# Optimization experiments

Hardware: AMD Instinct MI355X
Metric: run time of the kernel (lower is better)

Reference implementation:

```python
import jax, jax.numpy as jnp
import numpy as np

D_MODEL = 1024
NUM_HEADS = 16
DK = D_MODEL // NUM_HEADS
B, S = 2, 2048


def _init_w(key, out_f, in_f):
    std = 2.0 / (in_f + out_f) ** 0.5
    w = jax.random.truncated_normal(key, -3.0, 3.0, (out_f, in_f), dtype=jnp.float32)
    return w * std


def setup_inputs() -> dict:
    key = jax.random.key(0)
    kx, kq, kk, kv, ko = jax.random.split(key, 5)
    return {
        "x": jax.random.normal(kx, (B, S, D_MODEL), dtype=jnp.float32),
        "Wq": _init_w(kq, D_MODEL, D_MODEL),
        "Wk": _init_w(kk, D_MODEL, D_MODEL),
        "Wv": _init_w(kv, D_MODEL, D_MODEL),
        "Wo": _init_w(ko, D_MODEL, D_MODEL),
    }


def reference(x, Wq, Wk, Wv, Wo):
    b, s, _ = x.shape
    # Linear: einsum('... d_in, d_out d_in -> ... d_out')
    q = jnp.einsum("bsd,ed->bse", x, Wq)
    k = jnp.einsum("bsd,ed->bse", x, Wk)
    v = jnp.einsum("bsd,ed->bse", x, Wv)
    # split heads: [b, s, h*dk] -> [b, h, s, dk]
    q = q.reshape(b, s, NUM_HEADS, DK).transpose(0, 2, 1, 3)
    k = k.reshape(b, s, NUM_HEADS, DK).transpose(0, 2, 1, 3)
    v = v.reshape(b, s, NUM_HEADS, DK).transpose(0, 2, 1, 3)
    scores = jnp.einsum("bhqd,bhkd->bhqk", q, k) / (DK ** 0.5)
    causal = jnp.tril(jnp.ones((s, s), dtype=bool))
    scores = jnp.where(causal, scores, -jnp.inf)
    wei = jax.nn.softmax(scores, axis=-1)
    attn = jnp.einsum("bhqk,bhkd->bhqd", wei, v)
    attn = attn.transpose(0, 2, 1, 3).reshape(b, s, NUM_HEADS * DK)
    return jnp.einsum("bsd,ed->bse", attn, Wo)
```

## Files before the change

### kernel.cpp

```cpp
#include <hip/hip_runtime.h>
#include <hip/hip_bf16.h>
#include <math.h>

typedef __bf16 bf16;
typedef __attribute__((ext_vector_type(8))) __bf16 bf16x8;
typedef __attribute__((ext_vector_type(4))) __bf16 bf16x4;
typedef __attribute__((ext_vector_type(4))) float f32x4;

#define NHEAD 16
#define DKH 64
#define SEQ 2048
#define DMODEL 1024

__device__ __forceinline__ void gl_lds16(const void* g, void* lds) {
  __builtin_amdgcn_global_load_lds(
      (const __attribute__((address_space(1))) unsigned int*)g,
      (__attribute__((address_space(3))) unsigned int*)lds, 16, 0, 0);
}

__global__ void cvt5_kernel(const float* __restrict__ x, const float* __restrict__ wq,
                            const float* __restrict__ wk, const float* __restrict__ wv,
                            const float* __restrict__ wo, bf16* __restrict__ xb,
                            bf16* __restrict__ wqb, bf16* __restrict__ wkb,
                            bf16* __restrict__ wvb, bf16* __restrict__ wob) {
  int i = blockIdx.x * blockDim.x + threadIdx.x;
  const float* src; bf16* dst; int li;
  if (i < 1048576)      { src = x;  dst = xb;  li = i; }
  else if (i < 1310720) { src = wq; dst = wqb; li = i - 1048576; }
  else if (i < 1572864) { src = wk; dst = wkb; li = i - 1310720; }
  else if (i < 1835008) { src = wv; dst = wvb; li = i - 1572864; }
  else                  { src = wo; dst = wob; li = i - 1835008; }
  float4 v = ((const float4*)src)[li];
  bf16x4 o = { (bf16)v.x, (bf16)v.y, (bf16)v.z, (bf16)v.w };
  ((bf16x4*)dst)[li] = o;
}

template<int MODE>
__global__ __launch_bounds__(256) void gemm_nt(const bf16* __restrict__ A,
                                               const bf16* __restrict__ Bw,
                                               float* __restrict__ Cf,
                                               bf16* __restrict__ Cq,
                                               bf16* __restrict__ Ck,
                                               bf16* __restrict__ Cv,
                                               int M, int N, int K) {
  __shared__ __attribute__((aligned(16))) bf16 As[128 * 32];
  __shared__ __attribute__((aligned(16))) bf16 Bs[128 * 32];
  const int t = threadIdx.x;
  const int w = t >> 6, l = t & 63;
  const int wr = w >> 1, wc = w & 1;
  const int lin = blockIdx.y * gridDim.x + blockIdx.x;
  const int cpx = (gridDim.x * gridDim.y) >> 3;
  const int swz = (lin & 7) * cpx + (lin >> 3);
  const int tm = (swz / gridDim.x) * 128, tn = (swz % gridDim.x) * 128;
  const int srow = l >> 2, scol = (l & 3) * 8;
  const int c16 = l & 15, g4 = l >> 4;

  f32x4 acc[4][4];
#pragma unroll
  for (int i = 0; i < 4; ++i)
#pragma unroll
    for (int j = 0; j < 4; ++j) acc[i][j] = f32x4{0.f, 0.f, 0.f, 0.f};

  for (int k0 = 0; k0 < K; k0 += 32) {
#pragma unroll
    for (int j = 0; j < 2; ++j) {
      const int r0 = w * 32 + j * 16;
      gl_lds16(A + (size_t)(tm + r0 + srow) * K + k0 + scol, &As[r0 * 32]);
      gl_lds16(Bw + (size_t)(tn + r0 + srow) * K + k0 + scol, &Bs[r0 * 32]);
    }
    __syncthreads();
    bf16x8 af[4], bfr[4];
#pragma unroll
    for (int i = 0; i < 4; ++i)
      af[i] = *(const bf16x8*)&As[(wr * 64 + i * 16 + c16) * 32 + g4 * 8];
#pragma unroll
    for (int j = 0; j < 4; ++j)
      bfr[j] = *(const bf16x8*)&Bs[(wc * 64 + j * 16 + c16) * 32 + g4 * 8];
#pragma unroll
    for (int i = 0; i < 4; ++i)
#pragma unroll
      for (int j = 0; j < 4; ++j)
        acc[i][j] = __builtin_amdgcn_mfma_f32_16x16x32_bf16(af[i], bfr[j], acc[i][j], 0, 0, 0);
    __syncthreads();
  }

  const int which = tn >> 10;
#pragma unroll
  for (int i = 0; i < 4; ++i) {
    const int row0 = tm + wr * 64 + i * 16 + g4 * 4;
#pragma unroll
    for (int j = 0; j < 4; ++j) {
      const int col = tn + wc * 64 + j * 16 + c16;
      if (MODE == 0) {
#pragma unroll
        for (int r = 0; r < 4; ++r) Cf[(size_t)(row0 + r) * N + col] = acc[i][j][r];
      } else {
        const int lc = col & 1023;
        if (which == 2) {
          const int bb = row0 >> 11, s = row0 & 2047;
          const int hh = lc >> 6, dk = lc & 63;
          bf16x4 o = { (bf16)acc[i][j][0], (bf16)acc[i][j][1],
                       (bf16)acc[i][j][2], (bf16)acc[i][j][3] };
          *(bf16x4*)&Cv[((size_t)(bb * NHEAD + hh) * DKH + dk) * SEQ + s] = o;
        } else {
          bf16* dst = which ? Ck : Cq;
#pragma unroll
          for (int r = 0; r < 4; ++r)
            dst[(size_t)(row0 + r) * DMODEL + lc] = (bf16)acc[i][j][r];
        }
      }
    }
  }
}

__device__ __forceinline__ bf16x8 lds_frag(const bf16* T, int row, int gran) {
  return *(const bf16x8*)&T[row * 64 + ((gran ^ (row & 7)) << 3)];
}

__device__ __forceinline__ f32x4 vmax4(f32x4 a, f32x4 b) {
  return f32x4{ fmaxf(a[0], b[0]), fmaxf(a[1], b[1]),
                fmaxf(a[2], b[2]), fmaxf(a[3], b[3]) };
}

__global__ __launch_bounds__(256) void attn_kernel(const bf16* __restrict__ qb,
                                                   const bf16* __restrict__ kb,
                                                   const bf16* __restrict__ vT,
                                                   bf16* __restrict__ ob) {
  __shared__ __attribute__((aligned(16))) bf16 Kt[2][64 * 64];
  __shared__ __attribute__((aligned(16))) bf16 Vt[2][64 * 64];
  __shared__ __attribute__((aligned(16))) bf16 Pb[4][16 * 64];
  const int w = threadIdx.x >> 6, l = threadIdx.x & 63;
  const int lin = blockIdx.x;
  const int swz = (lin & 7) * 64 + (lin >> 3);
  const int pr = swz & 15, h = (swz >> 4) & 15, b = swz >> 8;
  const int qtA = 31 - pr, qtB = pr;
  const int c16 = l & 15, g4 = l >> 4, r8 = l >> 3;
  const int sg = ((l & 7) ^ (r8 & 7)) * 8;

  const float SC = 0.125f * 1.44269504089f;

  const bf16* kbase = kb + (size_t)b * SEQ * DMODEL + h * DKH;
  const bf16* vbase = vT + (size_t)(b * NHEAD + h) * DKH * SEQ;

  bf16x8 qfA[2], qfB[2];
#pragma unroll
  for (int d = 0; d < 2; ++d) {
    qfA[d] = *(const bf16x8*)(qb + (size_t)(b * SEQ + qtA * 64 + w * 16 + c16) * DMODEL +
                              h * DKH + d * 32 + g4 * 8);
    qfB[d] = *(const bf16x8*)(qb + (size_t)(b * SEQ + qtB * 64 + w * 16 + c16) * DMODEL +
                              h * DKH + d * 32 + g4 * 8);
  }

  auto stage = [&](int buf, int t) {
    const int kt0 = t * 64;
#pragma unroll
    for (int c = 0; c < 2; ++c) {
      const int row = w * 16 + c * 8;
      gl_lds16(kbase + (size_t)(kt0 + row + r8) * DMODEL + sg, &Kt[buf][row * 64]);
      gl_lds16(vbase + (size_t)(row + r8) * SEQ + kt0 + sg, &Vt[buf][row * 64]);
    }
  };

  stage(0, 0);
  __syncthreads();

  float mm = -INFINITY, ll = 0.f;
  f32x4 acc[4];
#pragma unroll
  for (int n = 0; n < 4; ++n) acc[n] = f32x4{0.f, 0.f, 0.f, 0.f};

  const int TA = qtA + 1, TT = TA + qtB + 1;
  const int ql = w * 16 + c16;

  for (int tt = 0; tt < TT; ++tt) {
    const int cur = tt & 1;
    if (tt + 1 < TT) stage(cur ^ 1, (tt + 1 < TA) ? tt + 1 : tt + 1 - TA);
    const bool pA = tt < TA;
    const int t_in = pA ? tt : tt - TA;
    const bool diag = (t_in == (pA ? qtA : qtB));
    const bf16x8 q0 = pA ? qfA[0] : qfB[0];
    const bf16x8 q1 = pA ? qfA[1] : qfB[1];

    f32x4 s[4];
    __builtin_amdgcn_s_setprio(1);
#pragma unroll
    for (int j = 0; j < 4; ++j) {
      bf16x8 kf0 = lds_frag(Kt[cur], j * 16 + c16, g4);
      bf16x8 kf1 = lds_frag(Kt[cur], j * 16 + c16, 4 + g4);
      f32x4 c = f32x4{0.f, 0.f, 0.f, 0.f};
      c = __builtin_amdgcn_mfma_f32_16x16x32_bf16(kf0, q0, c, 0, 0, 0);
      c = __builtin_amdgcn_mfma_f32_16x16x32_bf16(kf1, q1, c, 0, 0, 0);
      s[j] = c * SC;
    }
    __builtin_amdgcn_s_setprio(0);
    if (diag) {
#pragma unroll
      for (int j = 0; j < 4; ++j)
#pragma unroll
        for (int r = 0; r < 4; ++r)
          if (j * 16 + g4 * 4 + r > ql) s[j][r] = -INFINITY;
    }
    f32x4 t01 = vmax4(s[0], s[1]);
    f32x4 t23 = vmax4(s[2], s[3]);
    f32x4 tv = vmax4(t01, t23);
    float v = fmaxf(fmaxf(tv[0], tv[1]), fmaxf(tv[2], tv[3]));
    v = fmaxf(v, __shfl_xor(v, 16));
    v = fmaxf(v, __shfl_xor(v, 32));
    const float mn = fmaxf(mm, v);
    const float scl = __builtin_amdgcn_exp2f(mm - mn);
    f32x4 ps = f32x4{0.f, 0.f, 0.f, 0.f};
#pragma unroll
    for (int j = 0; j < 4; ++j)
#pragma unroll
      for (int r = 0; r < 4; ++r) {
        float p = __builtin_amdgcn_exp2f(s[j][r] - mn);
        s[j][r] = p;
        ps[r] += p;
      }
    float rs = (ps[0] + ps[1]) + (ps[2] + ps[3]);
    rs += __shfl_xor(rs, 16);
    rs += __shfl_xor(rs, 32);
    ll = ll * scl + rs;
    mm = mn;
    bf16* P = &Pb[w][0];
#pragma unroll
    for (int j = 0; j < 4; ++j) {
      const int col = j * 16 + g4 * 4;
      bf16x4 pk = { (bf16)s[j][0], (bf16)s[j][1], (bf16)s[j][2], (bf16)s[j][3] };
      *(bf16x4*)&P[c16 * 64 + (((col >> 3) ^ (c16 & 7)) << 3) + (col & 7)] = pk;
    }
    float sc4[4];
#pragma unroll
    for (int r = 0; r < 4; ++r) sc4[r] = __shfl(scl, g4 * 4 + r);
#pragma unroll
    for (int n = 0; n < 4; ++n)
#pragma unroll
      for (int r = 0; r < 4; ++r) acc[n][r] *= sc4[r];
    bf16x8 pa0 = lds_frag(P, c16, g4);
    bf16x8 pa1 = lds_frag(P, c16, 4 + g4);
    __builtin_amdgcn_s_setprio(1);
#pragma unroll
    for (int n = 0; n < 4; ++n) {
      bf16x8 vf0 = lds_frag(Vt[cur], n * 16 + c16, g4);
      bf16x8 vf1 = lds_frag(Vt[cur], n * 16 + c16, 4 + g4);
      acc[n] = __builtin_amdgcn_mfma_f32_16x16x32_bf16(pa0, vf0, acc[n], 0, 0, 0);
      acc[n] = __builtin_amdgcn_mfma_f32_16x16x32_bf16(pa1, vf1, acc[n], 0, 0, 0);
    }
    __builtin_amdgcn_s_setprio(0);

    if (tt == TA - 1) {
      float ls[4];
#pragma unroll
      for (int r = 0; r < 4; ++r) ls[r] = __shfl(ll, g4 * 4 + r);
#pragma unroll
      for (int n = 0; n < 4; ++n)
#pragma unroll
        for (int r = 0; r < 4; ++r) {
          float o = acc[n][r] / ls[r];
          ob[(size_t)(b * SEQ + qtA * 64 + w * 16 + g4 * 4 + r) * DMODEL +
             h * DKH + n * 16 + c16] = (bf16)o;
          acc[n][r] = 0.f;
        }
      mm = -INFINITY;
      ll = 0.f;
    }
    __syncthreads();
  }

  float ls[4];
#pragma unroll
  for (int r = 0; r < 4; ++r) ls[r] = __shfl(ll, g4 * 4 + r);
#pragma unroll
  for (int n = 0; n < 4; ++n)
#pragma unroll
    for (int r = 0; r < 4; ++r) {
      float o = acc[n][r] / ls[r];
      ob[(size_t)(b * SEQ + qtB * 64 + w * 16 + g4 * 4 + r) * DMODEL +
         h * DKH + n * 16 + c16] = (bf16)o;
    }
}

extern "C" void kernel_launch(void* const* d_in, const int* in_sizes, int n_in,
                              void* d_out, int out_size, void* d_ws, size_t ws_size,
                              hipStream_t stream) {
  const float* x  = (const float*)d_in[0];
  const float* Wq = (const float*)d_in[1];
  const float* Wk = (const float*)d_in[2];
  const float* Wv = (const float*)d_in[3];
  const float* Wo = (const float*)d_in[4];
  float* out = (float*)d_out;
  char* ws = (char*)d_ws;
  const size_t MB = (size_t)1 << 20;

  bf16* xb   = (bf16*)(ws + 0 * MB);
  bf16* wqb  = (bf16*)(ws + 8 * MB);
  bf16* wkb  = (bf16*)(ws + 10 * MB);
  bf16* wvb  = (bf16*)(ws + 12 * MB);
  bf16* wob  = (bf16*)(ws + 14 * MB);
  bf16* qbuf = (bf16*)(ws + 16 * MB);
  bf16* kbuf = (bf16*)(ws + 24 * MB);
  bf16* vTb  = (bf16*)(ws + 32 * MB);
  bf16* abuf = (bf16*)(ws + 40 * MB);

  cvt5_kernel<<<8192, 256, 0, stream>>>(x, Wq, Wk, Wv, Wo, xb, wqb, wkb, wvb, wob);

  gemm_nt<3><<<dim3(3072 / 128, 4096 / 128), 256, 0, stream>>>(
      xb, wqb, nullptr, qbuf, kbuf, vTb, 4096, 3072, 1024);

  attn_kernel<<<dim3(512), 256, 0, stream>>>(qbuf, kbuf, vTb, abuf);

  gemm_nt<0><<<dim3(1024 / 128, 4096 / 128), 256, 0, stream>>>(
      abuf, wob, out, nullptr, nullptr, nullptr, 4096, 1024, 1024);
}
```

Baseline: 194.9 us.

## Widen GEMM K-tile with swizzled LDS and add lazy softmax rescale with MFMA row sums

The GEMM K-step doubles to 64, and its LDS tiles use an XOR swizzle through the shared lds_frag helper. This halves the barrier count and should cut bank conflicts. The attention kernel folds the softmax scale into an FMA before exp2. It rescales the accumulator only when the running max grows past a threshold, checked once per wave. Row sums are computed by MFMA against a ones vector instead of by shuffle reductions, which trades VALU and shuffle work for extra matrix ops and bf16-rounded sums.

Result: faster. 181.8 us (-6.7%).

```diff
diff --git a/kernel.cpp b/kernel.cpp
--- a/kernel.cpp
+++ b/kernel.cpp
@@ -35,6 +35,10 @@
   ((bf16x4*)dst)[li] = o;
 }
 
+__device__ __forceinline__ bf16x8 lds_frag(const bf16* T, int row, int gran) {
+  return *(const bf16x8*)&T[row * 64 + ((gran ^ (row & 7)) << 3)];
+}
+
 template<int MODE>
 __global__ __launch_bounds__(256) void gemm_nt(const bf16* __restrict__ A,
                                                const bf16* __restrict__ Bw,
@@ -43,8 +47,8 @@
                                                bf16* __restrict__ Ck,
                                                bf16* __restrict__ Cv,
                                                int M, int N, int K) {
-  __shared__ __attribute__((aligned(16))) bf16 As[128 * 32];
-  __shared__ __attribute__((aligned(16))) bf16 Bs[128 * 32];
+  __shared__ __attribute__((aligned(16))) bf16 As[128 * 64];
+  __shared__ __attribute__((aligned(16))) bf16 Bs[128 * 64];
   const int t = threadIdx.x;
   const int w = t >> 6, l = t & 63;
   const int wr = w >> 1, wc = w & 1;
@@ -52,8 +56,8 @@
   const int cpx = (gridDim.x * gridDim.y) >> 3;
   const int swz = (lin & 7) * cpx + (lin >> 3);
   const int tm = (swz / gridDim.x) * 128, tn = (swz % gridDim.x) * 128;
-  const int srow = l >> 2, scol = (l & 3) * 8;
-  const int c16 = l & 15, g4 = l >> 4;
+  const int c16 = l & 15, g4 = l >> 4, r8 = l >> 3;
+  const int sg = ((l & 7) ^ (r8 & 7)) * 8;
 
   f32x4 acc[4][4];
 #pragma unroll
@@ -61,26 +65,29 @@
 #pragma unroll
     for (int j = 0; j < 4; ++j) acc[i][j] = f32x4{0.f, 0.f, 0.f, 0.f};
 
-  for (int k0 = 0; k0 < K; k0 += 32) {
-#pragma unroll
-    for (int j = 0; j < 2; ++j) {
-      const int r0 = w * 32 + j * 16;
-      gl_lds16(A + (size_t)(tm + r0 + srow) * K + k0 + scol, &As[r0 * 32]);
-      gl_lds16(Bw + (size_t)(tn + r0 + srow) * K + k0 + scol, &Bs[r0 * 32]);
+  for (int k0 = 0; k0 < K; k0 += 64) {
+#pragma unroll
+    for (int c = 0; c < 4; ++c) {
+      const int r0 = w * 32 + c * 8;
+      gl_lds16(A + (size_t)(tm + r0 + r8) * K + k0 + sg, &As[r0 * 64]);
+      gl_lds16(Bw + (size_t)(tn + r0 + r8) * K + k0 + sg, &Bs[r0 * 64]);
     }
     __syncthreads();
-    bf16x8 af[4], bfr[4];
-#pragma unroll
-    for (int i = 0; i < 4; ++i)
-      af[i] = *(const bf16x8*)&As[(wr * 64 + i * 16 + c16) * 32 + g4 * 8];
-#pragma unroll
-    for (int j = 0; j < 4; ++j)
-      bfr[j] = *(const bf16x8*)&Bs[(wc * 64 + j * 16 + c16) * 32 + g4 * 8];
-#pragma unroll
-    for (int i = 0; i < 4; ++i)
+#pragma unroll
+    for (int h = 0; h < 2; ++h) {
+      bf16x8 af[4], bfr[4];
+#pragma unroll
+      for (int i = 0; i < 4; ++i)
+        af[i] = lds_frag(As, wr * 64 + i * 16 + c16, h * 4 + g4);
 #pragma unroll
       for (int j = 0; j < 4; ++j)
-        acc[i][j] = __builtin_amdgcn_mfma_f32_16x16x32_bf16(af[i], bfr[j], acc[i][j], 0, 0, 0);
+        bfr[j] = lds_frag(Bs, wc * 64 + j * 16 + c16, h * 4 + g4);
+#pragma unroll
+      for (int i = 0; i < 4; ++i)
+#pragma unroll
+        for (int j = 0; j < 4; ++j)
+          acc[i][j] = __builtin_amdgcn_mfma_f32_16x16x32_bf16(af[i], bfr[j], acc[i][j], 0, 0, 0);
+    }
     __syncthreads();
   }
 
@@ -111,10 +118,6 @@
       }
     }
   }
-}
-
-__device__ __forceinline__ bf16x8 lds_frag(const bf16* T, int row, int gran) {
-  return *(const bf16x8*)&T[row * 64 + ((gran ^ (row & 7)) << 3)];
 }
 
 __device__ __forceinline__ f32x4 vmax4(f32x4 a, f32x4 b) {
@@ -137,7 +140,11 @@
   const int c16 = l & 15, g4 = l >> 4, r8 = l >> 3;
   const int sg = ((l & 7) ^ (r8 & 7)) * 8;
 
-  const float SC = 0.125f * 1.44269504089f;
+  const float SC2 = 0.125f * 1.44269504089f;
+  const float THR = 8.0f / SC2;
+
+  const bf16 oneb = (bf16)1.0f;
+  const bf16x8 ones = { oneb, oneb, oneb, oneb, oneb, oneb, oneb, oneb };
 
   const bf16* kbase = kb + (size_t)b * SEQ * DMODEL + h * DKH;
   const bf16* vbase = vT + (size_t)(b * NHEAD + h) * DKH * SEQ;
@@ -164,7 +171,8 @@
   stage(0, 0);
   __syncthreads();
 
-  float mm = -INFINITY, ll = 0.f;
+  float mm = -INFINITY;
+  f32x4 lsum4 = f32x4{0.f, 0.f, 0.f, 0.f};
   f32x4 acc[4];
 #pragma unroll
   for (int n = 0; n < 4; ++n) acc[n] = f32x4{0.f, 0.f, 0.f, 0.f};
@@ -190,7 +198,7 @@
       f32x4 c = f32x4{0.f, 0.f, 0.f, 0.f};
       c = __builtin_amdgcn_mfma_f32_16x16x32_bf16(kf0, q0, c, 0, 0, 0);
       c = __builtin_amdgcn_mfma_f32_16x16x32_bf16(kf1, q1, c, 0, 0, 0);
-      s[j] = c * SC;
+      s[j] = c;
     }
     __builtin_amdgcn_s_setprio(0);
     if (diag) {
@@ -206,36 +214,31 @@
     float v = fmaxf(fmaxf(tv[0], tv[1]), fmaxf(tv[2], tv[3]));
     v = fmaxf(v, __shfl_xor(v, 16));
     v = fmaxf(v, __shfl_xor(v, 32));
-    const float mn = fmaxf(mm, v);
-    const float scl = __builtin_amdgcn_exp2f(mm - mn);
-    f32x4 ps = f32x4{0.f, 0.f, 0.f, 0.f};
-#pragma unroll
-    for (int j = 0; j < 4; ++j)
-#pragma unroll
-      for (int r = 0; r < 4; ++r) {
-        float p = __builtin_amdgcn_exp2f(s[j][r] - mn);
-        s[j][r] = p;
-        ps[r] += p;
-      }
-    float rs = (ps[0] + ps[1]) + (ps[2] + ps[3]);
-    rs += __shfl_xor(rs, 16);
-    rs += __shfl_xor(rs, 32);
-    ll = ll * scl + rs;
-    mm = mn;
+    if (!__all(v <= mm + THR)) {
+      const float mn = fmaxf(mm, v);
+      const float scl = __builtin_amdgcn_exp2f(SC2 * (mm - mn));
+      float sc4[4];
+#pragma unroll
+      for (int r = 0; r < 4; ++r) sc4[r] = __shfl(scl, g4 * 4 + r);
+#pragma unroll
+      for (int n = 0; n < 4; ++n)
+#pragma unroll
+        for (int r = 0; r < 4; ++r) acc[n][r] *= sc4[r];
+#pragma unroll
+      for (int r = 0; r < 4; ++r) lsum4[r] *= sc4[r];
+      mm = mn;
+    }
+    const float nb = SC2 * mm;
     bf16* P = &Pb[w][0];
 #pragma unroll
     for (int j = 0; j < 4; ++j) {
+      bf16x4 pk;
+#pragma unroll
+      for (int r = 0; r < 4; ++r)
+        pk[r] = (bf16)__builtin_amdgcn_exp2f(fmaf(s[j][r], SC2, -nb));
       const int col = j * 16 + g4 * 4;
-      bf16x4 pk = { (bf16)s[j][0], (bf16)s[j][1], (bf16)s[j][2], (bf16)s[j][3] };
       *(bf16x4*)&P[c16 * 64 + (((col >> 3) ^ (c16 & 7)) << 3) + (col & 7)] = pk;
     }
-    float sc4[4];
-#pragma unroll
-    for (int r = 0; r < 4; ++r) sc4[r] = __shfl(scl, g4 * 4 + r);
-#pragma unroll
-    for (int n = 0; n < 4; ++n)
-#pragma unroll
-      for (int r = 0; r < 4; ++r) acc[n][r] *= sc4[r];
     bf16x8 pa0 = lds_frag(P, c16, g4);
     bf16x8 pa1 = lds_frag(P, c16, 4 + g4);
     __builtin_amdgcn_s_setprio(1);
@@ -246,35 +249,31 @@
       acc[n] = __builtin_amdgcn_mfma_f32_16x16x32_bf16(pa0, vf0, acc[n], 0, 0, 0);
       acc[n] = __builtin_amdgcn_mfma_f32_16x16x32_bf16(pa1, vf1, acc[n], 0, 0, 0);
     }
+    lsum4 = __builtin_amdgcn_mfma_f32_16x16x32_bf16(pa0, ones, lsum4, 0, 0, 0);
+    lsum4 = __builtin_amdgcn_mfma_f32_16x16x32_bf16(pa1, ones, lsum4, 0, 0, 0);
     __builtin_amdgcn_s_setprio(0);
 
     if (tt == TA - 1) {
-      float ls[4];
-#pragma unroll
-      for (int r = 0; r < 4; ++r) ls[r] = __shfl(ll, g4 * 4 + r);
 #pragma unroll
       for (int n = 0; n < 4; ++n)
 #pragma unroll
         for (int r = 0; r < 4; ++r) {
-          float o = acc[n][r] / ls[r];
+          float o = acc[n][r] / lsum4[r];
           ob[(size_t)(b * SEQ + qtA * 64 + w * 16 + g4 * 4 + r) * DMODEL +
              h * DKH + n * 16 + c16] = (bf16)o;
           acc[n][r] = 0.f;
         }
+      lsum4 = f32x4{0.f, 0.f, 0.f, 0.f};
       mm = -INFINITY;
-      ll = 0.f;
     }
     __syncthreads();
   }
 
-  float ls[4];
-#pragma unroll
-  for (int r = 0; r < 4; ++r) ls[r] = __shfl(ll, g4 * 4 + r);
 #pragma unroll
   for (int n = 0; n < 4; ++n)
 #pragma unroll
     for (int r = 0; r < 4; ++r) {
-      float o = acc[n][r] / ls[r];
+      float o = acc[n][r] / lsum4[r];
       ob[(size_t)(b * SEQ + qtB * 64 + w * 16 + g4 * 4 + r) * DMODEL +
          h * DKH + n * 16 + c16] = (bf16)o;
     }
```
